# Performance work log

Measured on AMD Instinct MI355X. Metric: run time of the kernel, lower is better.

The kernel has to match this reference:

```python
import jax, jax.numpy as jnp
import numpy as np

D_MODEL = 1024
NUM_HEADS = 16
HEAD_DIM = D_MODEL // NUM_HEADS
B, S = 4, 2048


def setup_inputs() -> dict:
    key = jax.random.key(0)
    ks = jax.random.split(key, 11)
    scale = 1.0 / np.sqrt(D_MODEL)
    return {
        "query": jax.random.normal(ks[0], (B, S, D_MODEL), jnp.float32),
        "key": jax.random.normal(ks[1], (B, S, D_MODEL), jnp.float32),
        "value": jax.random.normal(ks[2], (B, S, D_MODEL), jnp.float32),
        "Wq": jax.random.normal(ks[3], (D_MODEL, D_MODEL), jnp.float32) * scale,
        "bq": jnp.zeros((D_MODEL,), jnp.float32),
        "Wk": jax.random.normal(ks[4], (D_MODEL, D_MODEL), jnp.float32) * scale,
        "bk": jnp.zeros((D_MODEL,), jnp.float32),
        "Wv": jax.random.normal(ks[5], (D_MODEL, D_MODEL), jnp.float32) * scale,
        "bv": jnp.zeros((D_MODEL,), jnp.float32),
        "Wo": jax.random.normal(ks[6], (D_MODEL, D_MODEL), jnp.float32) * scale,
        "bo": jnp.zeros((D_MODEL,), jnp.float32),
    }


def reference(query, key, value, Wq, bq, Wk, bk, Wv, bv, Wo, bo):
    b = query.shape[0]
    # nn.Linear: x @ W.T + b; weights stored [out, in]
    def split_heads(x):
        return x.reshape(b, -1, NUM_HEADS, HEAD_DIM).transpose(0, 2, 1, 3)  # [b,h,s,d]
    q = split_heads(query @ Wq.T + bq)
    k = split_heads(key @ Wk.T + bk)
    v = split_heads(value @ Wv.T + bv)
    scores = jnp.einsum("bhqd,bhkd->bhqk", q, k) / np.sqrt(HEAD_DIM)
    weights = jax.nn.softmax(scores, axis=-1)
    out = jnp.einsum("bhqk,bhkd->bhqd", weights, v)
    out = out.transpose(0, 2, 1, 3).reshape(b, -1, D_MODEL)
    return out @ Wo.T + bo
```

## Files before the change

### kernel.cpp

```cpp
#include <hip/hip_runtime.h>

typedef __bf16 bf16;
typedef __bf16 bf16x4 __attribute__((ext_vector_type(4)));
typedef __bf16 bf16x8 __attribute__((ext_vector_type(8)));
typedef float f32x4 __attribute__((ext_vector_type(4)));

#define MFMA16(a, b, c) __builtin_amdgcn_mfma_f32_16x16x32_bf16((a), (b), (c), 0, 0, 0)

#define QSCALE 0.1803368808f

__device__ __forceinline__ void async_cp16(const bf16* g, bf16* l) {
    __builtin_amdgcn_global_load_lds((const __attribute__((address_space(1))) void*)g,
                                     (__attribute__((address_space(3))) void*)l, 16, 0, 0);
}

struct CvtArgs { const float* src[7]; bf16* dst[7]; };
__global__ void cvt_all(CvtArgs a) {
    int bx = blockIdx.x, t, off;
    if (bx < 12288) { t = bx >> 12;            off = bx & 4095; }
    else            { t = 3 + ((bx - 12288) >> 9); off = (bx - 12288) & 511; }
    size_t i = (size_t)off * 256 + threadIdx.x;
    const float4* p = (const float4*)(a.src[t] + i * 8);
    float4 x = p[0], y = p[1];
    bf16x8 o;
    o[0] = (bf16)x.x; o[1] = (bf16)x.y; o[2] = (bf16)x.z; o[3] = (bf16)x.w;
    o[4] = (bf16)y.x; o[5] = (bf16)y.y; o[6] = (bf16)y.z; o[7] = (bf16)y.w;
    *(bf16x8*)(a.dst[t] + i * 8) = o;
}

__device__ __forceinline__ void gemm_core(
    const bf16* __restrict__ A, const bf16* __restrict__ W,
    const float* __restrict__ bias, void* __restrict__ Cout,
    int mode, int m0, int n0)
{
    __shared__ bf16 As[128 * 64];
    __shared__ bf16 Bs[128 * 64];
    const int K = 1024;
    const int tid = threadIdx.x;
    const int lane = tid & 63, wave = tid >> 6;
    const int l15 = lane & 15, quad = lane >> 4, l7 = l15 & 7;
    const int wm = wave >> 1, wn = wave & 1;

    f32x4 acc[4][4] = {};

    const int rb = tid >> 3;
    const int cg8 = ((tid & 7) ^ (rb & 7)) * 8;
    const bf16* Ag = A + (size_t)(m0 + rb) * K + cg8;
    const bf16* Wg = W + (size_t)(n0 + rb) * K + cg8;
    bf16* Al = As + tid * 8;
    bf16* Bl = Bs + tid * 8;

    for (int k0 = 0; k0 < K; k0 += 64) {
        __syncthreads();
#pragma unroll
        for (int j = 0; j < 4; ++j) {
            async_cp16(Ag + k0 + (size_t)(j * 32) * K, Al + j * 2048);
            async_cp16(Wg + k0 + (size_t)(j * 32) * K, Bl + j * 2048);
        }
        __syncthreads();

#pragma unroll
        for (int ks = 0; ks < 2; ++ks) {
            bf16x8 af[4], bfr[4];
#pragma unroll
            for (int t = 0; t < 4; ++t) {
                const int sw = ((ks * 4 + quad) ^ l7) * 8;
                af[t]  = *(const bf16x8*)(As + (wm * 64 + t * 16 + l15) * 64 + sw);
                bfr[t] = *(const bf16x8*)(Bs + (wn * 64 + t * 16 + l15) * 64 + sw);
            }
#pragma unroll
            for (int mt = 0; mt < 4; ++mt)
#pragma unroll
                for (int nt = 0; nt < 4; ++nt)
                    acc[mt][nt] = MFMA16(af[mt], bfr[nt], acc[mt][nt]);
        }
    }

#pragma unroll
    for (int mt = 0; mt < 4; ++mt) {
#pragma unroll
        for (int nt = 0; nt < 4; ++nt) {
            int col = n0 + wn * 64 + nt * 16 + l15;
            float bcol = (mode == 2) ? 0.0f : bias[col];
#pragma unroll
            for (int r = 0; r < 4; ++r) {
                int row = m0 + wm * 64 + mt * 16 + quad * 4 + r;
                float val = acc[mt][nt][r];
                if (mode == 2) {
                    val += bias[row];
                    int bb = col >> 11, s = col & 2047;
                    int u = s & 31;
                    int sp = (s & ~31) | (((u >> 2) & 3) * 8 + (u >> 4) * 4 + (u & 3));
                    ((bf16*)Cout)[((size_t)(bb * 1024 + row) << 11) + sp] = (bf16)val;
                } else if (mode == 3) {
                    ((float*)Cout)[(size_t)row * 1024 + col] = val + bcol;
                } else {
                    val += bcol;
                    if (mode == 0) val *= QSCALE;
                    int bb = row >> 11, s = row & 2047, hh = col >> 6, d = col & 63;
                    ((bf16*)Cout)[(((size_t)(bb * 16 + hh) * 2048 + s) << 6) + d] = (bf16)val;
                }
            }
        }
    }
}

struct QkvArgs {
    const bf16* A[3];
    const bf16* W[3];
    const float* bias[3];
    bf16* out[3];
};

__global__ __launch_bounds__(256) void qkv_gemm(QkvArgs t) {
    int z = blockIdx.y;
    int bx = blockIdx.x;
    int m0, n0;
    if (z < 2) { m0 = (bx & 63) * 128; n0 = (bx >> 6) * 128; }
    else       { m0 = (bx & 7) * 128;  n0 = (bx >> 3) * 128; }
    gemm_core(t.A[z], t.W[z], t.bias[z], t.out[z], z, m0, n0);
}

__global__ __launch_bounds__(256) void oproj_gemm(
    const bf16* __restrict__ A, const bf16* __restrict__ W,
    const float* __restrict__ bias, float* __restrict__ Cout) {
    gemm_core(A, W, bias, Cout, 3, blockIdx.x * 128, blockIdx.y * 128);
}

__global__ __launch_bounds__(256, 2) void attn_kernel(
    const bf16* __restrict__ Qh, const bf16* __restrict__ Kh,
    const bf16* __restrict__ Vtg, bf16* __restrict__ AO)
{
    __shared__ bf16 Kl[64 * 64];
    __shared__ bf16 Vl[64 * 64];

    const int tid = threadIdx.x;
    const int lane = tid & 63, wave = tid >> 6;
    const int l15 = lane & 15, quad = lane >> 4, l7 = l15 & 7;
    const int h = blockIdx.y, b = blockIdx.z;
    const size_t base = (size_t)(b * 16 + h) << 17;
    const int q0 = blockIdx.x * 256 + wave * 64;

    bf16x8 qf[4][2];
#pragma unroll
    for (int qt = 0; qt < 4; ++qt)
#pragma unroll
        for (int ks = 0; ks < 2; ++ks)
            qf[qt][ks] = *(const bf16x8*)(Qh + base + (q0 + qt * 16 + l15) * 64 + ks * 32 + quad * 8);

    f32x4 o[4][4] = {};
    float ls[4] = {};

    const int sr = tid >> 3;
    const int sc0 = ((tid & 7) ^ (sr & 7)) * 8;
    const int sr2 = sr + 32;

    for (int kt = 0; kt < 2048; kt += 64) {
        __syncthreads();
        async_cp16(Kh + base + (size_t)(kt + sr) * 64 + sc0, Kl + tid * 8);
        async_cp16(Kh + base + (size_t)(kt + sr2) * 64 + sc0, Kl + (tid + 256) * 8);
        async_cp16(Vtg + base + (size_t)sr * 2048 + kt + sc0, Vl + tid * 8);
        async_cp16(Vtg + base + (size_t)sr2 * 2048 + kt + sc0, Vl + (tid + 256) * 8);
        __syncthreads();

        bf16x8 kb[2][4];
#pragma unroll
        for (int ks = 0; ks < 2; ++ks)
#pragma unroll
            for (int ktile = 0; ktile < 4; ++ktile)
                kb[ks][ktile] = *(const bf16x8*)(Kl + (ktile * 16 + l15) * 64 + (((ks * 4 + quad) ^ l7) * 8));

        bf16x8 pf[4][2];
#pragma unroll
        for (int qt = 0; qt < 4; ++qt) {
            f32x4 sc[4] = {};
#pragma unroll
            for (int ks = 0; ks < 2; ++ks)
#pragma unroll
                for (int ktile = 0; ktile < 4; ++ktile)
                    sc[ktile] = MFMA16(kb[ks][ktile], qf[qt][ks], sc[ktile]);
            float sum = 0.0f;
#pragma unroll
            for (int kc = 0; kc < 2; ++kc) {
                bf16x8 pk;
#pragma unroll
                for (int t = 0; t < 2; ++t)
#pragma unroll
                    for (int r = 0; r < 4; ++r) {
                        float p = __builtin_amdgcn_exp2f(sc[kc * 2 + t][r]);
                        sum += p;
                        pk[t * 4 + r] = (bf16)p;
                    }
                pf[qt][kc] = pk;
            }
            ls[qt] += sum;
        }

        bf16x8 va[4][2];
#pragma unroll
        for (int dt = 0; dt < 4; ++dt)
#pragma unroll
            for (int kc = 0; kc < 2; ++kc)
                va[dt][kc] = *(const bf16x8*)(Vl + (dt * 16 + l15) * 64 + (((kc * 4 + quad) ^ l7) * 8));

#pragma unroll
        for (int dt = 0; dt < 4; ++dt)
#pragma unroll
            for (int qt = 0; qt < 4; ++qt)
#pragma unroll
                for (int kc = 0; kc < 2; ++kc)
                    o[dt][qt] = MFMA16(va[dt][kc], pf[qt][kc], o[dt][qt]);
    }

#pragma unroll
    for (int qt = 0; qt < 4; ++qt) {
        float l = ls[qt];
        l += __shfl_xor(l, 16, 64);
        l += __shfl_xor(l, 32, 64);
        float inv = 1.0f / l;
        size_t rb = ((size_t)(b * 2048 + q0 + qt * 16 + l15)) * 1024 + h * 64;
#pragma unroll
        for (int dt = 0; dt < 4; ++dt) {
            bf16x4 ov = {(bf16)(o[dt][qt][0] * inv), (bf16)(o[dt][qt][1] * inv),
                         (bf16)(o[dt][qt][2] * inv), (bf16)(o[dt][qt][3] * inv)};
            *(bf16x4*)(AO + rb + dt * 16 + quad * 4) = ov;
        }
    }
}

extern "C" void kernel_launch(void* const* d_in, const int* in_sizes, int n_in,
                              void* d_out, int out_size, void* d_ws, size_t ws_size,
                              hipStream_t stream) {
    const float* q  = (const float*)d_in[0];
    const float* k  = (const float*)d_in[1];
    const float* v  = (const float*)d_in[2];
    const float* Wq = (const float*)d_in[3];
    const float* bq = (const float*)d_in[4];
    const float* Wk = (const float*)d_in[5];
    const float* bk = (const float*)d_in[6];
    const float* Wv = (const float*)d_in[7];
    const float* bv = (const float*)d_in[8];
    const float* Wo = (const float*)d_in[9];
    const float* bo = (const float*)d_in[10];
    float* out = (float*)d_out;

    const size_t NX = (size_t)8192 * 1024;
    const size_t NW = (size_t)1024 * 1024;
    bf16* ws  = (bf16*)d_ws;
    bf16* Xq  = ws;
    bf16* Xk  = Xq + NX;
    bf16* Xv  = Xk + NX;
    bf16* Wqb = Xv + NX;
    bf16* Wkb = Wqb + NW;
    bf16* Wvb = Wkb + NW;
    bf16* Wob = Wvb + NW;
    bf16* Qh  = Wob + NW;
    bf16* Kh  = Qh + NX;
    bf16* Vt  = Kh + NX;
    bf16* AO  = Xq;

    CvtArgs ca;
    ca.src[0] = q;  ca.dst[0] = Xq;
    ca.src[1] = k;  ca.dst[1] = Xk;
    ca.src[2] = v;  ca.dst[2] = Xv;
    ca.src[3] = Wq; ca.dst[3] = Wqb;
    ca.src[4] = Wk; ca.dst[4] = Wkb;
    ca.src[5] = Wv; ca.dst[5] = Wvb;
    ca.src[6] = Wo; ca.dst[6] = Wob;
    cvt_all<<<14336, 256, 0, stream>>>(ca);

    dim3 bb(256, 1, 1);
    QkvArgs t;
    t.A[0] = Xq;  t.W[0] = Wqb; t.bias[0] = bq; t.out[0] = Qh;
    t.A[1] = Xk;  t.W[1] = Wkb; t.bias[1] = bk; t.out[1] = Kh;
    t.A[2] = Wvb; t.W[2] = Xv;  t.bias[2] = bv; t.out[2] = Vt;
    qkv_gemm<<<dim3(512, 3), bb, 0, stream>>>(t);

    attn_kernel<<<dim3(8, 16, 4), bb, 0, stream>>>(Qh, Kh, Vt, AO);

    oproj_gemm<<<dim3(64, 8), bb, 0, stream>>>(AO, Wob, bo, out);
}
```

Baseline: 340.7 us.

## Rewrite GEMMs as 256x256 tiles with 5-stage async LDS pipeline

Replaces the 128x128 single-buffered GEMM core with a 256x256-tile, 512-thread kernel that uses a five-buffer rotating LDS ring fed by async global-to-LDS loads. It overlaps loads with MFMA compute using explicit vmcnt waits, barriers and setprio. It also remaps block indices so consecutive blocks are spread across XCDs. The goal is to raise arithmetic intensity and hide memory latency in the QKV and output projections. The cost is 160KB of LDS per block and many more accumulator registers, which may limit occupancy to one block per CU despite the launch bounds.

```diff
diff --git a/kernel.cpp b/kernel.cpp
--- a/kernel.cpp
+++ b/kernel.cpp
@@ -28,63 +28,90 @@
     *(bf16x8*)(a.dst[t] + i * 8) = o;
 }
 
-__device__ __forceinline__ void gemm_core(
+__device__ __forceinline__ void gemm256(
     const bf16* __restrict__ A, const bf16* __restrict__ W,
     const float* __restrict__ bias, void* __restrict__ Cout,
     int mode, int m0, int n0)
 {
-    __shared__ bf16 As[128 * 64];
-    __shared__ bf16 Bs[128 * 64];
+    __shared__ bf16 lds[81920];
     const int K = 1024;
     const int tid = threadIdx.x;
     const int lane = tid & 63, wave = tid >> 6;
-    const int l15 = lane & 15, quad = lane >> 4, l7 = l15 & 7;
-    const int wm = wave >> 1, wn = wave & 1;
-
-    f32x4 acc[4][4] = {};
-
-    const int rb = tid >> 3;
-    const int cg8 = ((tid & 7) ^ (rb & 7)) * 8;
-    const bf16* Ag = A + (size_t)(m0 + rb) * K + cg8;
-    const bf16* Wg = W + (size_t)(n0 + rb) * K + cg8;
-    bf16* Al = As + tid * 8;
-    bf16* Bl = Bs + tid * 8;
-
-    for (int k0 = 0; k0 < K; k0 += 64) {
-        __syncthreads();
-#pragma unroll
-        for (int j = 0; j < 4; ++j) {
-            async_cp16(Ag + k0 + (size_t)(j * 32) * K, Al + j * 2048);
-            async_cp16(Wg + k0 + (size_t)(j * 32) * K, Bl + j * 2048);
-        }
-        __syncthreads();
-
-#pragma unroll
-        for (int ks = 0; ks < 2; ++ks) {
-            bf16x8 af[4], bfr[4];
-#pragma unroll
-            for (int t = 0; t < 4; ++t) {
-                const int sw = ((ks * 4 + quad) ^ l7) * 8;
-                af[t]  = *(const bf16x8*)(As + (wm * 64 + t * 16 + l15) * 64 + sw);
-                bfr[t] = *(const bf16x8*)(Bs + (wn * 64 + t * 16 + l15) * 64 + sw);
-            }
-#pragma unroll
-            for (int mt = 0; mt < 4; ++mt)
-#pragma unroll
-                for (int nt = 0; nt < 4; ++nt)
-                    acc[mt][nt] = MFMA16(af[mt], bfr[nt], acc[mt][nt]);
-        }
+    const int l15 = lane & 15, quad = lane >> 4;
+    const int wm = wave >> 2, wn = wave & 3;
+
+    f32x4 acc[8][4] = {};
+
+    const int rA = tid >> 2;
+    const int cg8 = ((tid & 3) ^ (rA & 3)) * 8;
+    const bf16* Ag0 = A + (size_t)(m0 + rA) * K + cg8;
+    const bf16* Ag1 = A + (size_t)(m0 + rA + 128) * K + cg8;
+    const bf16* Bg0 = W + (size_t)(n0 + rA) * K + cg8;
+    const bf16* Bg1 = W + (size_t)(n0 + rA + 128) * K + cg8;
+
+    auto stage = [&](int u, int k0) {
+        bf16* p = lds + u;
+        async_cp16(Ag0 + k0, p + tid * 8);
+        async_cp16(Ag1 + k0, p + (tid + 512) * 8);
+        async_cp16(Bg0 + k0, p + 8192 + tid * 8);
+        async_cp16(Bg1 + k0, p + 8192 + (tid + 512) * 8);
+    };
+
+    const int csw = (quad ^ (l15 & 3)) * 8;
+    int afo[8], bfo[4];
+#pragma unroll
+    for (int mt = 0; mt < 8; ++mt) afo[mt] = (wm * 128 + mt * 16 + l15) * 32 + csw;
+#pragma unroll
+    for (int nt = 0; nt < 4; ++nt) bfo[nt] = 8192 + (wn * 64 + nt * 16 + l15) * 32 + csw;
+
+    auto phase = [&](int cu, int su, int k0s, bool doStage, int vmsel) {
+        bf16x8 af[8], bf[4];
+#pragma unroll
+        for (int mt = 0; mt < 8; ++mt) af[mt] = *(const bf16x8*)(lds + cu + afo[mt]);
+#pragma unroll
+        for (int nt = 0; nt < 4; ++nt) bf[nt] = *(const bf16x8*)(lds + cu + bfo[nt]);
+        if (doStage) stage(su, k0s);
+        __builtin_amdgcn_s_barrier();
+        asm volatile("s_waitcnt lgkmcnt(0)" ::: "memory");
+        __builtin_amdgcn_sched_barrier(0);
+        __builtin_amdgcn_s_setprio(1);
+#pragma unroll
+        for (int mt = 0; mt < 8; ++mt)
+#pragma unroll
+            for (int nt = 0; nt < 4; ++nt)
+                acc[mt][nt] = MFMA16(af[mt], bf[nt], acc[mt][nt]);
+        __builtin_amdgcn_s_setprio(0);
+        if (vmsel == 2)      asm volatile("s_waitcnt vmcnt(8)" ::: "memory");
+        else if (vmsel == 1) asm volatile("s_waitcnt vmcnt(4)" ::: "memory");
+        else if (vmsel == 0) asm volatile("s_waitcnt vmcnt(0)" ::: "memory");
+        if (vmsel >= 0) __builtin_amdgcn_s_barrier();
+    };
+
+    int r0 = 0, r1 = 16384, r2 = 32768, r3 = 49152, r4 = 65536;
+    auto rot = [&]() { int tmp = r0; r0 = r1; r1 = r2; r2 = r3; r3 = r4; r4 = tmp; };
+
+    stage(r0, 0); stage(r1, 32); stage(r2, 64);
+    asm volatile("s_waitcnt vmcnt(8)" ::: "memory");
+    __builtin_amdgcn_s_barrier();
+
+    for (int t = 0; t < 14; ++t) {
+        phase(r0, r3, (2 * t + 3) * 32, true, 2); rot();
+        phase(r0, r3, (2 * t + 4) * 32, true, 2); rot();
     }
-
-#pragma unroll
-    for (int mt = 0; mt < 4; ++mt) {
+    phase(r0, r3, 31 * 32, true, 2); rot();
+    phase(r0, 0, 0, false, 1); rot();
+    phase(r0, 0, 0, false, 0); rot();
+    phase(r0, 0, 0, false, -1);
+
+#pragma unroll
+    for (int mt = 0; mt < 8; ++mt) {
 #pragma unroll
         for (int nt = 0; nt < 4; ++nt) {
             int col = n0 + wn * 64 + nt * 16 + l15;
             float bcol = (mode == 2) ? 0.0f : bias[col];
 #pragma unroll
             for (int r = 0; r < 4; ++r) {
-                int row = m0 + wm * 64 + mt * 16 + quad * 4 + r;
+                int row = m0 + wm * 128 + mt * 16 + quad * 4 + r;
                 float val = acc[mt][nt][r];
                 if (mode == 2) {
                     val += bias[row];
@@ -112,19 +139,22 @@
     bf16* out[3];
 };
 
-__global__ __launch_bounds__(256) void qkv_gemm(QkvArgs t) {
-    int z = blockIdx.y;
-    int bx = blockIdx.x;
+__global__ __launch_bounds__(512, 2) void qkv_gemm(QkvArgs t) {
+    int bid = blockIdx.x;
+    int idx = (bid & 7) * 48 + (bid >> 3);
+    int z = idx >> 7, r = idx & 127;
     int m0, n0;
-    if (z < 2) { m0 = (bx & 63) * 128; n0 = (bx >> 6) * 128; }
-    else       { m0 = (bx & 7) * 128;  n0 = (bx >> 3) * 128; }
-    gemm_core(t.A[z], t.W[z], t.bias[z], t.out[z], z, m0, n0);
-}
-
-__global__ __launch_bounds__(256) void oproj_gemm(
+    if (z < 2) { m0 = (r >> 2) * 256; n0 = (r & 3) * 256; }
+    else       { m0 = (r >> 5) * 256; n0 = (r & 31) * 256; }
+    gemm256(t.A[z], t.W[z], t.bias[z], t.out[z], z, m0, n0);
+}
+
+__global__ __launch_bounds__(512, 2) void oproj_gemm(
     const bf16* __restrict__ A, const bf16* __restrict__ W,
     const float* __restrict__ bias, float* __restrict__ Cout) {
-    gemm_core(A, W, bias, Cout, 3, blockIdx.x * 128, blockIdx.y * 128);
+    int bid = blockIdx.x;
+    int idx = (bid & 7) * 16 + (bid >> 3);
+    gemm256(A, W, bias, Cout, 3, (idx >> 2) * 256, (idx & 3) * 256);
 }
 
 __global__ __launch_bounds__(256, 2) void attn_kernel(
@@ -269,14 +299,13 @@
     ca.src[6] = Wo; ca.dst[6] = Wob;
     cvt_all<<<14336, 256, 0, stream>>>(ca);
 
-    dim3 bb(256, 1, 1);
     QkvArgs t;
     t.A[0] = Xq;  t.W[0] = Wqb; t.bias[0] = bq; t.out[0] = Qh;
     t.A[1] = Xk;  t.W[1] = Wkb; t.bias[1] = bk; t.out[1] = Kh;
     t.A[2] = Wvb; t.W[2] = Xv;  t.bias[2] = bv; t.out[2] = Vt;
-    qkv_gemm<<<dim3(512, 3), bb, 0, stream>>>(t);
-
-    attn_kernel<<<dim3(8, 16, 4), bb, 0, stream>>>(Qh, Kh, Vt, AO);
-
-    oproj_gemm<<<dim3(64, 8), bb, 0, stream>>>(AO, Wob, bo, out);
-}
+    qkv_gemm<<<384, 512, 0, stream>>>(t);
+
+    attn_kernel<<<dim3(8, 16, 4), dim3(256, 1, 1), 0, stream>>>(Qh, Kh, Vt, AO);
+
+    oproj_gemm<<<128, 512, 0, stream>>>(AO, Wob, bo, out);
+}
```

Result: slower. 365.4 us (+7.2%).
